# Performance work log

Measured on AMD Instinct MI355X. Metric: run time of the kernel, lower is better.

The kernel has to match this reference:

```python
import jax, jax.numpy as jnp
import numpy as np

TOP_K = 2
ROUTED_SCALE = 1.0


def setup_inputs() -> dict:
    key = jax.random.key(0)
    ks = jax.random.split(key, 8)
    B, S, H, I, E, NS = 2, 1024, 768, 3072, 8, 2
    w = lambda k, shape: jax.random.normal(k, shape, jnp.float32) * 0.02
    return {
        "hidden_states": jax.random.normal(ks[0], (B, S, H), jnp.float32),
        "gate_w": w(ks[1], (E, H)),            # router gate: Linear(H->E, no bias), weight [out,in]
        "shared_gate": w(ks[2], (NS, I, H)),   # stacked shared-expert gate_proj weights
        "shared_up": w(ks[3], (NS, I, H)),
        "shared_down": w(ks[4], (NS, H, I)),
        "routed_gate": w(ks[5], (E, I, H)),    # stacked routed-expert weights
        "routed_up": w(ks[6], (E, I, H)),
        "routed_down": w(ks[7], (E, H, I)),
    }


def _swiglu_all(x, gw, uw, dw):
    """Run all stacked SwiGLU experts on all tokens.
    x: [T,H]; gw,uw: [E,I,H]; dw: [E,H,I] -> [T,E,H]"""
    g = jnp.einsum('th,eih->tei', x, gw)
    u = jnp.einsum('th,eih->tei', x, uw)
    h = jax.nn.silu(g) * u
    return jnp.einsum('tei,ehi->teh', h, dw)


def reference(hidden_states, gate_w, shared_gate, shared_up, shared_down,
              routed_gate, routed_up, routed_down):
    B, S, H = hidden_states.shape
    T = B * S
    x = hidden_states.reshape(T, H)

    # ---- Router (token choice, softmax scoring, no capacity/bias) ----
    router_logits = x @ gate_w.T                      # [T, E]
    scores = jax.nn.softmax(router_logits, axis=-1)   # [T, E]
    _, topk_idx = jax.lax.top_k(scores, TOP_K)        # [T, k]
    topk_w = jnp.take_along_axis(scores, topk_idx, axis=-1)
    topk_w = topk_w / (topk_w.sum(axis=-1, keepdims=True) + 1e-8)
    topk_w = topk_w * ROUTED_SCALE                    # [T, k]

    # Combine matrix: weight for each (token, expert); 0 if not selected.
    E = gate_w.shape[0]
    combine = jnp.zeros((T, E), scores.dtype).at[
        jnp.arange(T)[:, None], topk_idx].add(topk_w)  # [T, E]

    # ---- Routed experts (dense-all-experts, masked combine == dispatch) ----
    routed_all = _swiglu_all(x, routed_gate, routed_up, routed_down)  # [T,E,H]
    routed_out = jnp.einsum('teh,te->th', routed_all, combine)        # [T, H]

    # ---- Shared experts: sum over shared experts / N_shared ----
    NS = shared_gate.shape[0]
    shared_all = _swiglu_all(x, shared_gate, shared_up, shared_down)  # [T,NS,H]
    shared_out = shared_all.sum(axis=1) / NS                          # [T, H]

    out = (shared_out + routed_out).reshape(B, S, H)
    return out
```

## Files before the change

### kernel.cpp

```cpp
#include <hip/hip_runtime.h>
#include <stdint.h>

typedef __attribute__((ext_vector_type(8))) short short8;
typedef __attribute__((ext_vector_type(4))) float f32x4;
typedef __attribute__((ext_vector_type(4))) unsigned short usvec4;

static constexpr int T_ = 2048;
static constexpr int H_ = 768;
static constexpr int I_ = 3072;
static constexpr int RCAP = 6144;
static constexpr int RT_ = RCAP + 2 * T_;
static constexpr int TILE_ = 128;
static constexpr int BK_ = 32;

static constexpr long WE_SG = 0;
static constexpr long WE_SU = 4718592;
static constexpr long WE_SD = 9437184;
static constexpr long WE_RG = 14155776;
static constexpr long WE_RU = 33030144;
static constexpr long WE_RD = 51904512;
static constexpr long OFF_XP   = 141557760;
static constexpr long OFF_HACT = 157286400;
static constexpr long OFF_PART = 220200960;
static constexpr long OFF_META = 245366784;
static constexpr long OFF_TIDX = 245367040;
static constexpr long OFF_TW   = 245383424;
static constexpr long OFF_TOK  = 245399808;
static constexpr long OFF_SLOT = 245440768;
static constexpr long OFF_WL   = 245481728;

__device__ __forceinline__ unsigned short f2bf(float f) {
  union { float f; unsigned u; } v; v.f = f;
  unsigned r = (v.u + 0x7FFFu + ((v.u >> 16) & 1u)) >> 16;
  return (unsigned short)r;
}

__device__ __forceinline__ void gload_lds16(const void* g, void* l) {
  typedef const __attribute__((address_space(1))) void gvoid;
  typedef __attribute__((address_space(3))) void lvoid;
  gvoid* gp = (gvoid*)(uintptr_t)g;
  lvoid* lp = (lvoid*)(uint32_t)(uintptr_t)l;
  __builtin_amdgcn_global_load_lds(gp, lp, 16, 0, 0);
}

__device__ __forceinline__ f32x4 mfma16(short8 a, short8 b, f32x4 c) {
  return __builtin_amdgcn_mfma_f32_16x16x32_bf16(a, b, c, 0, 0, 0);
}

__device__ __forceinline__ short8 ds_read_b128_asm(unsigned int addr) {
  short8 v;
  asm volatile("ds_read_b128 %0, %1" : "=v"(v) : "v"(addr));
  return v;
}

__device__ __forceinline__ void wait_lgkm0_fence() {
  asm volatile("s_waitcnt lgkmcnt(0)" ::: "memory");
  __builtin_amdgcn_sched_barrier(0);
}
__device__ __forceinline__ void wait_vmcnt_barrier6(bool counted) {
  if (counted) asm volatile("s_waitcnt vmcnt(6)" ::: "memory");
  else         asm volatile("s_waitcnt vmcnt(0)" ::: "memory");
  __builtin_amdgcn_s_barrier();
  __builtin_amdgcn_sched_barrier(0);
}
__device__ __forceinline__ void wait_vmcnt_barrier4(bool counted) {
  if (counted) asm volatile("s_waitcnt vmcnt(4)" ::: "memory");
  else         asm volatile("s_waitcnt vmcnt(0)" ::: "memory");
  __builtin_amdgcn_s_barrier();
  __builtin_amdgcn_sched_barrier(0);
}

__device__ __forceinline__ unsigned swz(unsigned o) {
  return o ^ (((o >> 7) & 3u) << 4);
}

__global__ void cast_weights_k(const float* __restrict__ sg, const float* __restrict__ su,
                               const float* __restrict__ sd, const float* __restrict__ rg,
                               const float* __restrict__ ru, const float* __restrict__ rd,
                               unsigned short* __restrict__ wb) {
  long c = (long)blockIdx.x * 256 + threadIdx.x;
  const float* src; long dstoff, lc; int dtype = 0;
  if      (c <  1179648) { src = sg; dstoff = WE_SG; lc = c; }
  else if (c <  2359296) { src = su; dstoff = WE_SU; lc = c - 1179648; }
  else if (c <  3538944) { src = sd; dstoff = WE_SD; lc = c - 2359296; dtype = 1; }
  else if (c <  8257536) { src = rg; dstoff = WE_RG; lc = c - 3538944; }
  else if (c < 12976128) { src = ru; dstoff = WE_RU; lc = c - 8257536; }
  else                   { src = rd; dstoff = WE_RD; lc = c - 12976128; dtype = 1; }
  f32x4 a = ((const f32x4*)src)[lc];
  usvec4 o;
  #pragma unroll
  for (int j = 0; j < 4; j++) o[j] = f2bf(a[j]);
  constexpr long EW = (long)I_ * H_;
  long f = lc * 4;
  long e = f / EW; f -= e * EW;
  long dst;
  if (dtype == 0) {
    int i = (int)(f / H_), h = (int)(f - (long)i * H_);
    dst = dstoff + e * EW + ((long)((i >> 7) * 24 + (h >> 5))) * 4096 + ((i & 127) << 5) + (h & 31);
  } else {
    int h = (int)(f / I_), i = (int)(f - (long)h * I_);
    dst = dstoff + e * EW + ((long)((h >> 7) * 96 + (i >> 5))) * 4096 + ((h & 127) << 5) + (i & 31);
  }
  *(usvec4*)(wb + dst) = o;
}

__global__ void router_k(const float* __restrict__ x, const float* __restrict__ gw,
                         int* __restrict__ tidx, float* __restrict__ tw) {
  const int lane = threadIdx.x & 63;
  const int wv = threadIdx.x >> 6;
  const int t = blockIdx.x * 4 + wv;
  float xv[12];
  #pragma unroll
  for (int j = 0; j < 12; j++) xv[j] = x[(long)t * H_ + lane + j * 64];
  float lg[8];
  #pragma unroll
  for (int e = 0; e < 8; e++) {
    float s = 0.f;
    #pragma unroll
    for (int j = 0; j < 12; j++) s += xv[j] * gw[e * H_ + lane + j * 64];
    #pragma unroll
    for (int o = 32; o > 0; o >>= 1) s += __shfl_xor(s, o, 64);
    lg[e] = s;
  }
  if (lane == 0) {
    float m = lg[0];
    #pragma unroll
    for (int e = 1; e < 8; e++) m = fmaxf(m, lg[e]);
    float ex[8]; float S = 0.f;
    #pragma unroll
    for (int e = 0; e < 8; e++) { ex[e] = __expf(lg[e] - m); S += ex[e]; }
    int i0 = 0;
    #pragma unroll
    for (int e = 1; e < 8; e++) if (ex[e] > ex[i0]) i0 = e;
    int i1 = (i0 == 0) ? 1 : 0;
    #pragma unroll
    for (int e = 0; e < 8; e++) if (e != i0 && ex[e] > ex[i1]) i1 = e;
    float s0 = ex[i0] / S, s1 = ex[i1] / S;
    float den = s0 + s1 + 1e-8f;
    tidx[t * 2] = i0; tidx[t * 2 + 1] = i1;
    tw[t * 2] = s0 / den; tw[t * 2 + 1] = s1 / den;
  }
}

__global__ void pack_k(const int* __restrict__ tidx, const float* __restrict__ tw,
                       int* __restrict__ meta, int* __restrict__ tokL,
                       int* __restrict__ slotL, float* __restrict__ wL) {
  __shared__ int cnt[8], base_s[8], cur[8];
  const int tid = threadIdx.x;
  if (tid < 8) { cnt[tid] = 0; cur[tid] = 0; }
  for (int r = tid; r < RT_; r += 1024) tokL[r] = -1;
  __syncthreads();
  for (int t = tid; t < T_; t += 1024) {
    atomicAdd(&cnt[tidx[t * 2]], 1);
    atomicAdd(&cnt[tidx[t * 2 + 1]], 1);
  }
  __syncthreads();
  if (tid == 0) {
    int run = 0;
    for (int e = 0; e < 8; e++) {
      base_s[e] = run;
      int pad = (cnt[e] + 127) & ~127;
      meta[e] = run;
      meta[10 + e] = pad;
      run += pad;
    }
    for (int s = 0; s < 2; s++) { meta[8 + s] = RCAP + s * T_; meta[18 + s] = T_; }
  }
  __syncthreads();
  for (int t = tid; t < T_; t += 1024) {
    for (int k = 0; k < 2; k++) {
      int e = tidx[t * 2 + k];
      int p = atomicAdd(&cur[e], 1);
      int R = base_s[e] + p;
      tokL[R] = t; slotL[R] = k; wL[R] = tw[t * 2 + k];
    }
    for (int s = 0; s < 2; s++) {
      int R = RCAP + s * T_ + t;
      tokL[R] = t; slotL[R] = 2 + s; wL[R] = 0.5f;
    }
  }
}

__global__ void gather_k(const float* __restrict__ x, const int* __restrict__ tokL,
                         unsigned short* __restrict__ xp) {
  const int r = blockIdx.x, tid = threadIdx.x;
  const int tok = tokL[r];
  const int c = tid * 4;
  usvec4 o = 0;
  if (tok >= 0) {
    f32x4 v = *(const f32x4*)(x + (long)tok * H_ + c);
    #pragma unroll
    for (int j = 0; j < 4; j++) o[j] = f2bf(v[j]);
  }
  long dst = ((long)(r >> 7) * 24 + (c >> 5)) * 4096 + ((r & 127) << 5) + (c & 31);
  *(usvec4*)(xp + dst) = o;
}

__global__ __launch_bounds__(256, 2)
void gemm1_k(const unsigned short* __restrict__ xp,
             const unsigned short* __restrict__ wb,
             const int* __restrict__ meta,
             unsigned short* __restrict__ hact) {
  const int fid = blockIdx.x;
  const int x   = fid & 7;
  const int q   = fid >> 3;
  const int bx  = q & 15;
  const int g   = (q >> 4) * 8 + x;
  const int e   = g / 24;
  const int by  = g % 24;

  const int rowsP = meta[10 + e];
  if (bx * TILE_ >= rowsP) return;
  const int base = meta[e];
  const int n0 = by * TILE_;

  const unsigned short* gwp;
  const unsigned short* uwp;
  if (e < 8) { gwp = wb + WE_RG + (long)e * I_ * H_;       uwp = wb + WE_RU + (long)e * I_ * H_; }
  else       { gwp = wb + WE_SG + (long)(e - 8) * I_ * H_; uwp = wb + WE_SU + (long)(e - 8) * I_ * H_; }

  const int rblk = (base >> 7) + bx;
  const char* aT = (const char*)(xp + (long)rblk * 24 * 4096);
  const char* gT = (const char*)(gwp + (long)by * 24 * 4096);
  const char* uT = (const char*)(uwp + (long)by * 24 * 4096);

  __shared__ alignas(16) unsigned short As[3 * TILE_ * BK_];
  __shared__ alignas(16) unsigned short Bg[3 * TILE_ * BK_];
  __shared__ alignas(16) unsigned short Bu[3 * TILE_ * BK_];

  const int tid = threadIdx.x;
  const unsigned o1 = tid * 16, o2 = 4096 + tid * 16;
  const unsigned s1 = swz(o1), s2 = swz(o2);

  const int lane = tid & 63, wv = tid >> 6;
  const int wm = wv >> 1, wn = wv & 1;
  const int lm = lane & 15, ld = lane >> 4;

  int aOff[4], bOff[4];
  #pragma unroll
  for (int i = 0; i < 4; i++) {
    int ra = wm * 64 + i * 16 + lm;
    int rb = wn * 64 + i * 16 + lm;
    aOff[i] = ra * 64 + ((ld * 16) ^ (((ra >> 1) & 3) << 4));
    bOff[i] = rb * 64 + ((ld * 16) ^ (((rb >> 1) & 3) << 4));
  }
  const unsigned asBase = (unsigned)(uintptr_t)As;
  const unsigned bgBase = (unsigned)(uintptr_t)Bg;
  const unsigned buBase = (unsigned)(uintptr_t)Bu;

  f32x4 accG[4][4] = {};
  f32x4 accU[4][4] = {};

  auto stage = [&](int buf, int kk) {
    const long ko = (long)kk * 8192;
    const unsigned bo = buf * 8192;
    gload_lds16(aT + ko + s1, (char*)As + bo + o1);
    gload_lds16(aT + ko + s2, (char*)As + bo + o2);
    gload_lds16(gT + ko + s1, (char*)Bg + bo + o1);
    gload_lds16(gT + ko + s2, (char*)Bg + bo + o2);
    gload_lds16(uT + ko + s1, (char*)Bu + bo + o1);
    gload_lds16(uT + ko + s2, (char*)Bu + bo + o2);
  };

  constexpr int NK = H_ / BK_;
  stage(0, 0);
  stage(1, 1);
  asm volatile("s_waitcnt vmcnt(6)" ::: "memory");
  __builtin_amdgcn_s_barrier();
  __builtin_amdgcn_sched_barrier(0);

  for (int kk = 0; kk < NK; ++kk) {
    const int cur = kk % 3;
    const bool more = (kk + 2 < NK);
    if (more) stage((kk + 2) % 3, kk + 2);
    const unsigned bo = cur * 8192;
    short8 av[4], gv[4], uv[4];
    #pragma unroll
    for (int i = 0; i < 4; i++) {
      av[i] = ds_read_b128_asm(asBase + bo + aOff[i]);
      gv[i] = ds_read_b128_asm(bgBase + bo + bOff[i]);
      uv[i] = ds_read_b128_asm(buBase + bo + bOff[i]);
    }
    wait_lgkm0_fence();
    #pragma unroll
    for (int mi = 0; mi < 4; mi++)
      #pragma unroll
      for (int ni = 0; ni < 4; ni++) {
        accG[mi][ni] = mfma16(av[mi], gv[ni], accG[mi][ni]);
        accU[mi][ni] = mfma16(av[mi], uv[ni], accU[mi][ni]);
      }
    wait_vmcnt_barrier6(more);
  }

  unsigned short* ep = (wv < 2) ? (As + wv * 2048) : (Bg + (wv - 2) * 2048);
  #pragma unroll
  for (int half = 0; half < 2; half++) {
    #pragma unroll
    for (int mi2 = 0; mi2 < 2; mi2++) {
      int mi = half * 2 + mi2;
      #pragma unroll
      for (int ni = 0; ni < 4; ni++) {
        f32x4 g2 = accG[mi][ni], u = accU[mi][ni];
        #pragma unroll
        for (int j = 0; j < 4; j++) {
          float gvv = g2[j];
          float hv = gvv / (1.0f + __expf(-gvv)) * u[j];
          ep[(mi2 * 16 + ld * 4 + j) * 64 + ni * 16 + lm] = f2bf(hv);
        }
      }
    }
    __syncthreads();
    #pragma unroll
    for (int it = 0; it < 4; it++) {
      int r = it * 8 + (lane >> 3);
      int c8 = (lane & 7) * 8;
      short8 v = *(const short8*)(ep + r * 64 + c8);
      int R7 = wm * 64 + half * 32 + r;
      int C = n0 + wn * 64 + c8;
      long dst = ((long)rblk * 96 + (C >> 5)) * 4096 + (R7 << 5) + (C & 31);
      *(short8*)(hact + dst) = v;
    }
    __syncthreads();
  }
}

__global__ __launch_bounds__(256, 3)
void gemm2_k(const unsigned short* __restrict__ hact,
             const unsigned short* __restrict__ wb,
             const int* __restrict__ meta,
             const int* __restrict__ tokL,
             const int* __restrict__ slotL,
             const float* __restrict__ wLst,
             float* __restrict__ parts) {
  const int fid = blockIdx.x;
  const int x   = fid & 7;
  const int q   = fid >> 3;
  const int bx  = q & 15;
  const int g   = (q >> 4) * 8 + x;
  if (g >= 60) return;
  const int e   = g / 6;
  const int by  = g % 6;

  const int rowsP = meta[10 + e];
  if (bx * TILE_ >= rowsP) return;
  const int base = meta[e];
  const int n0 = by * TILE_;
  const unsigned short* dwp = (e < 8) ? wb + WE_RD + (long)e * H_ * I_
                                      : wb + WE_SD + (long)(e - 8) * H_ * I_;
  const int rblk = (base >> 7) + bx;
  const char* aT = (const char*)(hact + (long)rblk * 96 * 4096);
  const char* bT = (const char*)(dwp + (long)by * 96 * 4096);

  __shared__ alignas(16) unsigned short As[3 * TILE_ * BK_];
  __shared__ alignas(16) unsigned short Bd[3 * TILE_ * BK_];
  const int tid = threadIdx.x;
  const unsigned o1 = tid * 16, o2 = 4096 + tid * 16;
  const unsigned s1 = swz(o1), s2 = swz(o2);
  const int lane = tid & 63, wv = tid >> 6;
  const int wm = wv >> 1, wn = wv & 1;
  const int lm = lane & 15, ld = lane >> 4;
  int aOff[4], bOff[4];
  #pragma unroll
  for (int i = 0; i < 4; i++) {
    int ra = wm * 64 + i * 16 + lm;
    int rb = wn * 64 + i * 16 + lm;
    aOff[i] = ra * 64 + ((ld * 16) ^ (((ra >> 1) & 3) << 4));
    bOff[i] = rb * 64 + ((ld * 16) ^ (((rb >> 1) & 3) << 4));
  }
  const unsigned asBase = (unsigned)(uintptr_t)As;
  const unsigned bdBase = (unsigned)(uintptr_t)Bd;
  f32x4 acc[4][4] = {};

  auto stage = [&](int buf, int kk) {
    const long ko = (long)kk * 8192;
    const unsigned bo = buf * 8192;
    gload_lds16(aT + ko + s1, (char*)As + bo + o1);
    gload_lds16(aT + ko + s2, (char*)As + bo + o2);
    gload_lds16(bT + ko + s1, (char*)Bd + bo + o1);
    gload_lds16(bT + ko + s2, (char*)Bd + bo + o2);
  };

  constexpr int NK = I_ / BK_;
  stage(0, 0);
  stage(1, 1);
  asm volatile("s_waitcnt vmcnt(4)" ::: "memory");
  __builtin_amdgcn_s_barrier();
  __builtin_amdgcn_sched_barrier(0);

  for (int kk = 0; kk < NK; ++kk) {
    const int cur = kk % 3;
    const bool more = (kk + 2 < NK);
    if (more) stage((kk + 2) % 3, kk + 2);
    const unsigned bo = cur * 8192;
    short8 av[4], bv[4];
    #pragma unroll
    for (int i = 0; i < 4; i++) {
      av[i] = ds_read_b128_asm(asBase + bo + aOff[i]);
      bv[i] = ds_read_b128_asm(bdBase + bo + bOff[i]);
    }
    wait_lgkm0_fence();
    #pragma unroll
    for (int mi = 0; mi < 4; mi++)
      #pragma unroll
      for (int ni = 0; ni < 4; ni++)
        acc[mi][ni] = mfma16(av[mi], bv[ni], acc[mi][ni]);
    wait_vmcnt_barrier4(more);
  }

  const long R0 = base + bx * TILE_ + wm * 64;
  #pragma unroll
  for (int mi = 0; mi < 4; mi++) {
    #pragma unroll
    for (int j = 0; j < 4; j++) {
      long R = R0 + mi * 16 + ld * 4 + j;
      int tok = tokL[R];
      if (tok < 0) continue;
      float w = wLst[R];
      long obase = (long)slotL[R] * (T_ * H_) + (long)tok * H_ + n0 + wn * 64 + lm;
      #pragma unroll
      for (int ni = 0; ni < 4; ni++) {
        parts[obase + ni * 16] = w * acc[mi][ni][j];
      }
    }
  }
}

__global__ void final_k(const float* __restrict__ parts, float* __restrict__ out) {
  const int i = blockIdx.x * 256 + threadIdx.x;
  const int N4 = T_ * H_ / 4;
  const f32x4* p = (const f32x4*)parts;
  f32x4 s = p[i];
  s += p[N4 + i];
  s += p[2 * N4 + i];
  s += p[3 * N4 + i];
  ((f32x4*)out)[i] = s;
}

extern "C" void kernel_launch(void* const* d_in, const int* in_sizes, int n_in,
                              void* d_out, int out_size, void* d_ws, size_t ws_size,
                              hipStream_t stream) {
  (void)in_sizes; (void)n_in; (void)out_size; (void)ws_size;
  const float* x  = (const float*)d_in[0];
  const float* gw = (const float*)d_in[1];
  const float* sg = (const float*)d_in[2];
  const float* su = (const float*)d_in[3];
  const float* sd = (const float*)d_in[4];
  const float* rg = (const float*)d_in[5];
  const float* ru = (const float*)d_in[6];
  const float* rd = (const float*)d_in[7];

  char* ws = (char*)d_ws;
  unsigned short* wb   = (unsigned short*)ws;
  unsigned short* xp   = (unsigned short*)(ws + OFF_XP);
  unsigned short* ha   = (unsigned short*)(ws + OFF_HACT);
  float*          prt  = (float*)(ws + OFF_PART);
  int*            meta = (int*)(ws + OFF_META);
  int*            tidx = (int*)(ws + OFF_TIDX);
  float*          tw   = (float*)(ws + OFF_TW);
  int*            tokL = (int*)(ws + OFF_TOK);
  int*            slotL= (int*)(ws + OFF_SLOT);
  float*          wl   = (float*)(ws + OFF_WL);

  cast_weights_k<<<69120, 256, 0, stream>>>(sg, su, sd, rg, ru, rd, wb);
  router_k<<<512, 256, 0, stream>>>(x, gw, tidx, tw);
  pack_k<<<1, 1024, 0, stream>>>(tidx, tw, meta, tokL, slotL, wl);
  gather_k<<<RT_, 192, 0, stream>>>(x, tokL, xp);
  gemm1_k<<<3840, 256, 0, stream>>>(xp, wb, meta, ha);
  gemm2_k<<<1024, 256, 0, stream>>>(ha, wb, meta, tokL, slotL, wl, prt);
  final_k<<<1536, 256, 0, stream>>>(prt, (float*)d_out);
}
```

Before: 279.6 us.

## Fuse router into gate/up cast and overlap down-weight cast with gemm1

Merges the router kernel into the gate/up weight cast kernel as extra blocks, so one launch is removed. The down-projection weight cast moves into the gemm1 prologue: every gemm1 block, including those that exit early, converts a slice of the down weights before its own GEMM, so the cast overlaps with gemm1 compute. gemm1 also splits its LDS reads with a partial lgkmcnt wait, so the gate MFMAs start before the up-weight reads finish. The risk is extra register pressure and memory traffic in gemm1, which could hurt its occupancy.

```diff
diff --git a/kernel.cpp b/kernel.cpp
--- a/kernel.cpp
+++ b/kernel.cpp
@@ -74,41 +74,34 @@
   return o ^ (((o >> 7) & 3u) << 4);
 }
 
-__global__ void cast_weights_k(const float* __restrict__ sg, const float* __restrict__ su,
-                               const float* __restrict__ sd, const float* __restrict__ rg,
-                               const float* __restrict__ ru, const float* __restrict__ rd,
-                               unsigned short* __restrict__ wb) {
-  long c = (long)blockIdx.x * 256 + threadIdx.x;
-  const float* src; long dstoff, lc; int dtype = 0;
-  if      (c <  1179648) { src = sg; dstoff = WE_SG; lc = c; }
-  else if (c <  2359296) { src = su; dstoff = WE_SU; lc = c - 1179648; }
-  else if (c <  3538944) { src = sd; dstoff = WE_SD; lc = c - 2359296; dtype = 1; }
-  else if (c <  8257536) { src = rg; dstoff = WE_RG; lc = c - 3538944; }
-  else if (c < 12976128) { src = ru; dstoff = WE_RU; lc = c - 8257536; }
-  else                   { src = rd; dstoff = WE_RD; lc = c - 12976128; dtype = 1; }
-  f32x4 a = ((const f32x4*)src)[lc];
-  usvec4 o;
-  #pragma unroll
-  for (int j = 0; j < 4; j++) o[j] = f2bf(a[j]);
-  constexpr long EW = (long)I_ * H_;
-  long f = lc * 4;
-  long e = f / EW; f -= e * EW;
-  long dst;
-  if (dtype == 0) {
+__global__ void cast_gu_router_k(const float* __restrict__ sg, const float* __restrict__ su,
+                                 const float* __restrict__ rg, const float* __restrict__ ru,
+                                 const float* __restrict__ x, const float* __restrict__ gw,
+                                 int* __restrict__ tidx, float* __restrict__ tw,
+                                 unsigned short* __restrict__ wb) {
+  const int b = blockIdx.x;
+  if (b < 46080) {
+    long c = (long)b * 256 + threadIdx.x;
+    const float* src; long dstoff, lc;
+    if      (c <  1179648) { src = sg; dstoff = WE_SG; lc = c; }
+    else if (c <  2359296) { src = su; dstoff = WE_SU; lc = c - 1179648; }
+    else if (c <  7077888) { src = rg; dstoff = WE_RG; lc = c - 2359296; }
+    else                   { src = ru; dstoff = WE_RU; lc = c - 7077888; }
+    f32x4 a = ((const f32x4*)src)[lc];
+    usvec4 o;
+    #pragma unroll
+    for (int j = 0; j < 4; j++) o[j] = f2bf(a[j]);
+    constexpr long EW = (long)I_ * H_;
+    long f = lc * 4;
+    long e = f / EW; f -= e * EW;
     int i = (int)(f / H_), h = (int)(f - (long)i * H_);
-    dst = dstoff + e * EW + ((long)((i >> 7) * 24 + (h >> 5))) * 4096 + ((i & 127) << 5) + (h & 31);
-  } else {
-    int h = (int)(f / I_), i = (int)(f - (long)h * I_);
-    dst = dstoff + e * EW + ((long)((h >> 7) * 96 + (i >> 5))) * 4096 + ((h & 127) << 5) + (i & 31);
-  }
-  *(usvec4*)(wb + dst) = o;
-}
-
-__global__ void router_k(const float* __restrict__ x, const float* __restrict__ gw,
-                         int* __restrict__ tidx, float* __restrict__ tw) {
+    long dst = dstoff + e * EW + ((long)((i >> 7) * 24 + (h >> 5))) * 4096 + ((i & 127) << 5) + (h & 31);
+    *(usvec4*)(wb + dst) = o;
+    return;
+  }
   const int lane = threadIdx.x & 63;
   const int wv = threadIdx.x >> 6;
-  const int t = blockIdx.x * 4 + wv;
+  const int t = (b - 46080) * 4 + wv;
   float xv[12];
   #pragma unroll
   for (int j = 0; j < 12; j++) xv[j] = x[(long)t * H_ + lane + j * 64];
@@ -198,10 +191,37 @@
 
 __global__ __launch_bounds__(256, 2)
 void gemm1_k(const unsigned short* __restrict__ xp,
-             const unsigned short* __restrict__ wb,
+             unsigned short* __restrict__ wb,
+             const float* __restrict__ sdp, const float* __restrict__ rdp,
              const int* __restrict__ meta,
              unsigned short* __restrict__ hact) {
   const int fid = blockIdx.x;
+  const int tid = threadIdx.x;
+
+  {
+    constexpr long EW = (long)I_ * H_;
+    f32x4 a[6]; long dst[6];
+    #pragma unroll
+    for (int it = 0; it < 6; ++it) {
+      long c = (long)fid * 1536 + it * 256 + tid;
+      const float* src; long dstoff, lc;
+      if (c < 1179648) { src = sdp; dstoff = WE_SD; lc = c; }
+      else             { src = rdp; dstoff = WE_RD; lc = c - 1179648; }
+      a[it] = ((const f32x4*)src)[lc];
+      long f = lc * 4;
+      long e2 = f / EW; f -= e2 * EW;
+      int h = (int)(f / I_), i2 = (int)(f - (long)h * I_);
+      dst[it] = dstoff + e2 * EW + ((long)((h >> 7) * 96 + (i2 >> 5))) * 4096 + ((h & 127) << 5) + (i2 & 31);
+    }
+    #pragma unroll
+    for (int it = 0; it < 6; ++it) {
+      usvec4 o;
+      #pragma unroll
+      for (int j = 0; j < 4; j++) o[j] = f2bf(a[it][j]);
+      *(usvec4*)(wb + dst[it]) = o;
+    }
+  }
+
   const int x   = fid & 7;
   const int q   = fid >> 3;
   const int bx  = q & 15;
@@ -228,7 +248,6 @@
   __shared__ alignas(16) unsigned short Bg[3 * TILE_ * BK_];
   __shared__ alignas(16) unsigned short Bu[3 * TILE_ * BK_];
 
-  const int tid = threadIdx.x;
   const unsigned o1 = tid * 16, o2 = 4096 + tid * 16;
   const unsigned s1 = swz(o1), s2 = swz(o2);
 
@@ -276,19 +295,25 @@
     const unsigned bo = cur * 8192;
     short8 av[4], gv[4], uv[4];
     #pragma unroll
-    for (int i = 0; i < 4; i++) {
-      av[i] = ds_read_b128_asm(asBase + bo + aOff[i]);
-      gv[i] = ds_read_b128_asm(bgBase + bo + bOff[i]);
-      uv[i] = ds_read_b128_asm(buBase + bo + bOff[i]);
-    }
-    wait_lgkm0_fence();
+    for (int i = 0; i < 4; i++) av[i] = ds_read_b128_asm(asBase + bo + aOff[i]);
+    #pragma unroll
+    for (int i = 0; i < 4; i++) gv[i] = ds_read_b128_asm(bgBase + bo + bOff[i]);
+    #pragma unroll
+    for (int i = 0; i < 4; i++) uv[i] = ds_read_b128_asm(buBase + bo + bOff[i]);
+    asm volatile("s_waitcnt lgkmcnt(4)" ::: "memory");
+    __builtin_amdgcn_sched_barrier(0);
     #pragma unroll
     for (int mi = 0; mi < 4; mi++)
       #pragma unroll
-      for (int ni = 0; ni < 4; ni++) {
+      for (int ni = 0; ni < 4; ni++)
         accG[mi][ni] = mfma16(av[mi], gv[ni], accG[mi][ni]);
+    asm volatile("s_waitcnt lgkmcnt(0)" ::: "memory");
+    __builtin_amdgcn_sched_barrier(0);
+    #pragma unroll
+    for (int mi = 0; mi < 4; mi++)
+      #pragma unroll
+      for (int ni = 0; ni < 4; ni++)
         accU[mi][ni] = mfma16(av[mi], uv[ni], accU[mi][ni]);
-      }
     wait_vmcnt_barrier6(more);
   }
 
@@ -461,11 +486,10 @@
   int*            slotL= (int*)(ws + OFF_SLOT);
   float*          wl   = (float*)(ws + OFF_WL);
 
-  cast_weights_k<<<69120, 256, 0, stream>>>(sg, su, sd, rg, ru, rd, wb);
-  router_k<<<512, 256, 0, stream>>>(x, gw, tidx, tw);
+  cast_gu_router_k<<<46592, 256, 0, stream>>>(sg, su, rg, ru, x, gw, tidx, tw, wb);
   pack_k<<<1, 1024, 0, stream>>>(tidx, tw, meta, tokL, slotL, wl);
   gather_k<<<RT_, 192, 0, stream>>>(x, tokL, xp);
-  gemm1_k<<<3840, 256, 0, stream>>>(xp, wb, meta, ha);
+  gemm1_k<<<3840, 256, 0, stream>>>(xp, wb, sd, rd, meta, ha);
   gemm2_k<<<1024, 256, 0, stream>>>(ha, wb, meta, tokL, slotL, wl, prt);
   final_k<<<1536, 256, 0, stream>>>(prt, (float*)d_out);
 }
```

After: 276.7 us. No clear change (-1.0%).

## Enlarge GEMM tiles to 256 rows with 512-thread blocks and shared B loads

Applied to the files above, without the earlier changes.

Both expert GEMMs move from 128x128 tiles with 256 threads to 256x128 tiles with 512 threads (8 waves), so each weight tile loaded into LDS is reused across twice as many token rows. Expert row padding in the packer grows to 256 so the bigger tiles align with expert boundaries. The LDS layout is merged into a single buffer, and the gemm1 epilogue writes each wave's slice without the two-phase sync. This cuts weight traffic per output but adds padding waste for experts with few tokens, uses more LDS per block (96KB for gemm1), and launches fewer blocks, which may lower occupancy.

```diff
diff --git a/kernel.cpp b/kernel.cpp
--- a/kernel.cpp
+++ b/kernel.cpp
@@ -10,8 +10,6 @@
 static constexpr int I_ = 3072;
 static constexpr int RCAP = 6144;
 static constexpr int RT_ = RCAP + 2 * T_;
-static constexpr int TILE_ = 128;
-static constexpr int BK_ = 32;
 
 static constexpr long WE_SG = 0;
 static constexpr long WE_SU = 4718592;
@@ -57,14 +55,14 @@
   asm volatile("s_waitcnt lgkmcnt(0)" ::: "memory");
   __builtin_amdgcn_sched_barrier(0);
 }
-__device__ __forceinline__ void wait_vmcnt_barrier6(bool counted) {
-  if (counted) asm volatile("s_waitcnt vmcnt(6)" ::: "memory");
+__device__ __forceinline__ void wait_vmcnt_barrier4(bool counted) {
+  if (counted) asm volatile("s_waitcnt vmcnt(4)" ::: "memory");
   else         asm volatile("s_waitcnt vmcnt(0)" ::: "memory");
   __builtin_amdgcn_s_barrier();
   __builtin_amdgcn_sched_barrier(0);
 }
-__device__ __forceinline__ void wait_vmcnt_barrier4(bool counted) {
-  if (counted) asm volatile("s_waitcnt vmcnt(4)" ::: "memory");
+__device__ __forceinline__ void wait_vmcnt_barrier3(bool counted) {
+  if (counted) asm volatile("s_waitcnt vmcnt(3)" ::: "memory");
   else         asm volatile("s_waitcnt vmcnt(0)" ::: "memory");
   __builtin_amdgcn_s_barrier();
   __builtin_amdgcn_sched_barrier(0);
@@ -159,7 +157,7 @@
     int run = 0;
     for (int e = 0; e < 8; e++) {
       base_s[e] = run;
-      int pad = (cnt[e] + 127) & ~127;
+      int pad = (cnt[e] + 255) & ~255;
       meta[e] = run;
       meta[10 + e] = pad;
       run += pad;
@@ -196,7 +194,7 @@
   *(usvec4*)(xp + dst) = o;
 }
 
-__global__ __launch_bounds__(256, 2)
+__global__ __launch_bounds__(512, 2)
 void gemm1_k(const unsigned short* __restrict__ xp,
              const unsigned short* __restrict__ wb,
              const int* __restrict__ meta,
@@ -204,33 +202,33 @@
   const int fid = blockIdx.x;
   const int x   = fid & 7;
   const int q   = fid >> 3;
-  const int bx  = q & 15;
-  const int g   = (q >> 4) * 8 + x;
+  const int bx  = q & 7;
+  const int g   = (q >> 3) * 8 + x;
   const int e   = g / 24;
   const int by  = g % 24;
 
   const int rowsP = meta[10 + e];
-  if (bx * TILE_ >= rowsP) return;
+  if (bx * 256 >= rowsP) return;
   const int base = meta[e];
-  const int n0 = by * TILE_;
+  const int n0 = by * 128;
 
   const unsigned short* gwp;
   const unsigned short* uwp;
   if (e < 8) { gwp = wb + WE_RG + (long)e * I_ * H_;       uwp = wb + WE_RU + (long)e * I_ * H_; }
   else       { gwp = wb + WE_SG + (long)(e - 8) * I_ * H_; uwp = wb + WE_SU + (long)(e - 8) * I_ * H_; }
 
-  const int rblk = (base >> 7) + bx;
-  const char* aT = (const char*)(xp + (long)rblk * 24 * 4096);
-  const char* gT = (const char*)(gwp + (long)by * 24 * 4096);
-  const char* uT = (const char*)(uwp + (long)by * 24 * 4096);
-
-  __shared__ alignas(16) unsigned short As[3 * TILE_ * BK_];
-  __shared__ alignas(16) unsigned short Bg[3 * TILE_ * BK_];
-  __shared__ alignas(16) unsigned short Bu[3 * TILE_ * BK_];
+  const int rblk = (base >> 7) + bx * 2;
+  const char* aT0 = (const char*)(xp + (long)rblk * 24 * 4096);
+  const char* aT1 = (const char*)(xp + (long)(rblk + 1) * 24 * 4096);
+  const char* gT  = (const char*)(gwp + (long)by * 24 * 4096);
+  const char* uT  = (const char*)(uwp + (long)by * 24 * 4096);
+
+  __shared__ alignas(16) char LDS[98304];
+  const unsigned ldsBase = (unsigned)(uintptr_t)LDS;
 
   const int tid = threadIdx.x;
-  const unsigned o1 = tid * 16, o2 = 4096 + tid * 16;
-  const unsigned s1 = swz(o1), s2 = swz(o2);
+  const unsigned o1 = tid * 16;
+  const unsigned s1 = swz(o1);
 
   const int lane = tid & 63, wv = tid >> 6;
   const int wm = wv >> 1, wn = wv & 1;
@@ -244,28 +242,22 @@
     aOff[i] = ra * 64 + ((ld * 16) ^ (((ra >> 1) & 3) << 4));
     bOff[i] = rb * 64 + ((ld * 16) ^ (((rb >> 1) & 3) << 4));
   }
-  const unsigned asBase = (unsigned)(uintptr_t)As;
-  const unsigned bgBase = (unsigned)(uintptr_t)Bg;
-  const unsigned buBase = (unsigned)(uintptr_t)Bu;
 
   f32x4 accG[4][4] = {};
   f32x4 accU[4][4] = {};
 
   auto stage = [&](int buf, int kk) {
     const long ko = (long)kk * 8192;
-    const unsigned bo = buf * 8192;
-    gload_lds16(aT + ko + s1, (char*)As + bo + o1);
-    gload_lds16(aT + ko + s2, (char*)As + bo + o2);
-    gload_lds16(gT + ko + s1, (char*)Bg + bo + o1);
-    gload_lds16(gT + ko + s2, (char*)Bg + bo + o2);
-    gload_lds16(uT + ko + s1, (char*)Bu + bo + o1);
-    gload_lds16(uT + ko + s2, (char*)Bu + bo + o2);
+    gload_lds16(aT0 + ko + s1, LDS + buf * 16384 + o1);
+    gload_lds16(aT1 + ko + s1, LDS + buf * 16384 + 8192 + o1);
+    gload_lds16(gT + ko + s1, LDS + 49152 + buf * 8192 + o1);
+    gload_lds16(uT + ko + s1, LDS + 73728 + buf * 8192 + o1);
   };
 
-  constexpr int NK = H_ / BK_;
+  constexpr int NK = H_ / 32;
   stage(0, 0);
   stage(1, 1);
-  asm volatile("s_waitcnt vmcnt(6)" ::: "memory");
+  asm volatile("s_waitcnt vmcnt(4)" ::: "memory");
   __builtin_amdgcn_s_barrier();
   __builtin_amdgcn_sched_barrier(0);
 
@@ -273,13 +265,14 @@
     const int cur = kk % 3;
     const bool more = (kk + 2 < NK);
     if (more) stage((kk + 2) % 3, kk + 2);
-    const unsigned bo = cur * 8192;
+    const unsigned boA = cur * 16384;
+    const unsigned boB = cur * 8192;
     short8 av[4], gv[4], uv[4];
     #pragma unroll
     for (int i = 0; i < 4; i++) {
-      av[i] = ds_read_b128_asm(asBase + bo + aOff[i]);
-      gv[i] = ds_read_b128_asm(bgBase + bo + bOff[i]);
-      uv[i] = ds_read_b128_asm(buBase + bo + bOff[i]);
+      av[i] = ds_read_b128_asm(ldsBase + boA + aOff[i]);
+      gv[i] = ds_read_b128_asm(ldsBase + 49152 + boB + bOff[i]);
+      uv[i] = ds_read_b128_asm(ldsBase + 73728 + boB + bOff[i]);
     }
     wait_lgkm0_fence();
     #pragma unroll
@@ -289,42 +282,37 @@
         accG[mi][ni] = mfma16(av[mi], gv[ni], accG[mi][ni]);
         accU[mi][ni] = mfma16(av[mi], uv[ni], accU[mi][ni]);
       }
-    wait_vmcnt_barrier6(more);
-  }
-
-  unsigned short* ep = (wv < 2) ? (As + wv * 2048) : (Bg + (wv - 2) * 2048);
-  #pragma unroll
-  for (int half = 0; half < 2; half++) {
-    #pragma unroll
-    for (int mi2 = 0; mi2 < 2; mi2++) {
-      int mi = half * 2 + mi2;
+    wait_vmcnt_barrier4(more);
+  }
+
+  unsigned short* ep = (unsigned short*)(LDS + wv * 8192);
+  #pragma unroll
+  for (int mi = 0; mi < 4; mi++)
+    #pragma unroll
+    for (int ni = 0; ni < 4; ni++) {
+      f32x4 g2 = accG[mi][ni], u = accU[mi][ni];
       #pragma unroll
-      for (int ni = 0; ni < 4; ni++) {
-        f32x4 g2 = accG[mi][ni], u = accU[mi][ni];
-        #pragma unroll
-        for (int j = 0; j < 4; j++) {
-          float gvv = g2[j];
-          float hv = gvv / (1.0f + __expf(-gvv)) * u[j];
-          ep[(mi2 * 16 + ld * 4 + j) * 64 + ni * 16 + lm] = f2bf(hv);
-        }
+      for (int j = 0; j < 4; j++) {
+        float gvv = g2[j];
+        float hv = gvv / (1.0f + __expf(-gvv)) * u[j];
+        ep[(mi * 16 + ld * 4 + j) * 64 + ni * 16 + lm] = f2bf(hv);
       }
     }
-    __syncthreads();
-    #pragma unroll
-    for (int it = 0; it < 4; it++) {
-      int r = it * 8 + (lane >> 3);
-      int c8 = (lane & 7) * 8;
-      short8 v = *(const short8*)(ep + r * 64 + c8);
-      int R7 = wm * 64 + half * 32 + r;
-      int C = n0 + wn * 64 + c8;
-      long dst = ((long)rblk * 96 + (C >> 5)) * 4096 + (R7 << 5) + (C & 31);
-      *(short8*)(hact + dst) = v;
-    }
-    __syncthreads();
-  }
-}
-
-__global__ __launch_bounds__(256, 3)
+  const int rblkO = rblk + (wm >> 1);
+  const int R7b = (wm & 1) * 64;
+  #pragma unroll
+  for (int it = 0; it < 8; it++) {
+    int r = it * 8 + (lane >> 3);
+    int c8 = (lane & 7) * 8;
+    short8 v = *(const short8*)(ep + r * 64 + c8);
+    int R7 = R7b + r;
+    int C = n0 + wn * 64 + c8;
+    long dst = ((long)rblkO * 96 + (C >> 5)) * 4096 + (R7 << 5) + (C & 31);
+    *(short8*)(hact + dst) = v;
+  }
+}
+
+__global__ __launch_bounds__(512, 4)
 void gemm2_k(const unsigned short* __restrict__ hact,
              const unsigned short* __restrict__ wb,
              const int* __restrict__ meta,
@@ -335,27 +323,29 @@
   const int fid = blockIdx.x;
   const int x   = fid & 7;
   const int q   = fid >> 3;
-  const int bx  = q & 15;
-  const int g   = (q >> 4) * 8 + x;
+  const int bx  = q & 7;
+  const int g   = (q >> 3) * 8 + x;
   if (g >= 60) return;
   const int e   = g / 6;
   const int by  = g % 6;
 
   const int rowsP = meta[10 + e];
-  if (bx * TILE_ >= rowsP) return;
+  if (bx * 256 >= rowsP) return;
   const int base = meta[e];
-  const int n0 = by * TILE_;
+  const int n0 = by * 128;
   const unsigned short* dwp = (e < 8) ? wb + WE_RD + (long)e * H_ * I_
                                       : wb + WE_SD + (long)(e - 8) * H_ * I_;
-  const int rblk = (base >> 7) + bx;
-  const char* aT = (const char*)(hact + (long)rblk * 96 * 4096);
-  const char* bT = (const char*)(dwp + (long)by * 96 * 4096);
-
-  __shared__ alignas(16) unsigned short As[3 * TILE_ * BK_];
-  __shared__ alignas(16) unsigned short Bd[3 * TILE_ * BK_];
+  const int rblk = (base >> 7) + bx * 2;
+  const char* aT0 = (const char*)(hact + (long)rblk * 96 * 4096);
+  const char* aT1 = (const char*)(hact + (long)(rblk + 1) * 96 * 4096);
+  const char* bT  = (const char*)(dwp + (long)by * 96 * 4096);
+
+  __shared__ alignas(16) char LDS[73728];
+  const unsigned ldsBase = (unsigned)(uintptr_t)LDS;
+
   const int tid = threadIdx.x;
-  const unsigned o1 = tid * 16, o2 = 4096 + tid * 16;
-  const unsigned s1 = swz(o1), s2 = swz(o2);
+  const unsigned o1 = tid * 16;
+  const unsigned s1 = swz(o1);
   const int lane = tid & 63, wv = tid >> 6;
   const int wm = wv >> 1, wn = wv & 1;
   const int lm = lane & 15, ld = lane >> 4;
@@ -367,23 +357,19 @@
     aOff[i] = ra * 64 + ((ld * 16) ^ (((ra >> 1) & 3) << 4));
     bOff[i] = rb * 64 + ((ld * 16) ^ (((rb >> 1) & 3) << 4));
   }
-  const unsigned asBase = (unsigned)(uintptr_t)As;
-  const unsigned bdBase = (unsigned)(uintptr_t)Bd;
   f32x4 acc[4][4] = {};
 
   auto stage = [&](int buf, int kk) {
     const long ko = (long)kk * 8192;
-    const unsigned bo = buf * 8192;
-    gload_lds16(aT + ko + s1, (char*)As + bo + o1);
-    gload_lds16(aT + ko + s2, (char*)As + bo + o2);
-    gload_lds16(bT + ko + s1, (char*)Bd + bo + o1);
-    gload_lds16(bT + ko + s2, (char*)Bd + bo + o2);
+    gload_lds16(aT0 + ko + s1, LDS + buf * 16384 + o1);
+    gload_lds16(aT1 + ko + s1, LDS + buf * 16384 + 8192 + o1);
+    gload_lds16(bT + ko + s1, LDS + 49152 + buf * 8192 + o1);
   };
 
-  constexpr int NK = I_ / BK_;
+  constexpr int NK = I_ / 32;
   stage(0, 0);
   stage(1, 1);
-  asm volatile("s_waitcnt vmcnt(4)" ::: "memory");
+  asm volatile("s_waitcnt vmcnt(3)" ::: "memory");
   __builtin_amdgcn_s_barrier();
   __builtin_amdgcn_sched_barrier(0);
 
@@ -391,12 +377,13 @@
     const int cur = kk % 3;
     const bool more = (kk + 2 < NK);
     if (more) stage((kk + 2) % 3, kk + 2);
-    const unsigned bo = cur * 8192;
+    const unsigned boA = cur * 16384;
+    const unsigned boB = cur * 8192;
     short8 av[4], bv[4];
     #pragma unroll
     for (int i = 0; i < 4; i++) {
-      av[i] = ds_read_b128_asm(asBase + bo + aOff[i]);
-      bv[i] = ds_read_b128_asm(bdBase + bo + bOff[i]);
+      av[i] = ds_read_b128_asm(ldsBase + boA + aOff[i]);
+      bv[i] = ds_read_b128_asm(ldsBase + 49152 + boB + bOff[i]);
     }
     wait_lgkm0_fence();
     #pragma unroll
@@ -404,10 +391,10 @@
       #pragma unroll
       for (int ni = 0; ni < 4; ni++)
         acc[mi][ni] = mfma16(av[mi], bv[ni], acc[mi][ni]);
-    wait_vmcnt_barrier4(more);
-  }
-
-  const long R0 = base + bx * TILE_ + wm * 64;
+    wait_vmcnt_barrier3(more);
+  }
+
+  const long R0 = base + bx * 256 + wm * 64;
   #pragma unroll
   for (int mi = 0; mi < 4; mi++) {
     #pragma unroll
@@ -465,7 +452,7 @@
   router_k<<<512, 256, 0, stream>>>(x, gw, tidx, tw);
   pack_k<<<1, 1024, 0, stream>>>(tidx, tw, meta, tokL, slotL, wl);
   gather_k<<<RT_, 192, 0, stream>>>(x, tokL, xp);
-  gemm1_k<<<3840, 256, 0, stream>>>(xp, wb, meta, ha);
-  gemm2_k<<<1024, 256, 0, stream>>>(ha, wb, meta, tokL, slotL, wl, prt);
+  gemm1_k<<<1920, 512, 0, stream>>>(xp, wb, meta, ha);
+  gemm2_k<<<512, 512, 0, stream>>>(ha, wb, meta, tokL, slotL, wl, prt);
   final_k<<<1536, 256, 0, stream>>>(prt, (float*)d_out);
 }
```

New measurement: 309.8 us. 10.8% more time.
